# Kernel optimization log

Measured on AMD Instinct MI355X. Metric: run time of the kernel, lower is better.

## Reference

```python
import jax, jax.numpy as jnp
import numpy as np

N_LAYERS = 8
WIDTH = 1024
N = N_LAYERS * WIDTH


def setup_inputs() -> dict:
    key = jax.random.key(0)
    k1, k2 = jax.random.split(key)
    x = jax.random.normal(k1, (WIDTH,), dtype=jnp.float32)
    # parameter_matrix: row i = weights over all N neurons + bias in column N
    params = jax.random.normal(k2, (N, N + 1), dtype=jnp.float32) * 0.1
    # Layered DAG adjacency: layer l -> layer l+1 fully connected.
    adj_np = np.zeros((N, N), dtype=bool)
    for l in range(N_LAYERS - 1):
        adj_np[l * WIDTH:(l + 1) * WIDTH, (l + 1) * WIDTH:(l + 2) * WIDTH] = True
    return {"x": x, "params": params, "adj": jnp.asarray(adj_np)}


def reference(x, params, adj):
    """Faithful forward of connex NeuralNetwork with dropout_p=0.

    values starts at zero; input neurons (ids 0..W-1) are set to x.
    Each topological batch (= layer here) fires via the dense masked
    dot-product the original uses: dot(params[i,:N], values*adj[:,i]) + bias.
    Hidden neurons use silu, output neurons use identity.
    """
    n = params.shape[0]
    w = x.shape[0]
    n_layers = n // w
    values = jnp.zeros((n,), dtype=x.dtype).at[:w].set(x)
    for l in range(1, n_layers):  # static loop over topo batches
        lo, hi = l * w, (l + 1) * w
        mask = adj[:, lo:hi].T                      # (w, n) incoming-edge mask
        masked = jnp.where(mask, values[None, :], 0.0)
        pre = jnp.einsum('wn,wn->w', params[lo:hi, :n], masked) + params[lo:hi, n]
        out = pre if l == n_layers - 1 else jax.nn.silu(pre)  # output_activation = identity
        values = values.at[lo:hi].set(out)
    return values[-w:]
```

## Files before the change

### kernel.cpp

```cpp
#include <hip/hip_runtime.h>
#include <hip/hip_cooperative_groups.h>
#include <math.h>

#define W_    1024
#define NL_   8
#define NTOT_ (W_ * NL_)
#define RS_   (NTOT_ + 1)
#define NBLK  256

#define WS_BARRIER_OFF 2048

__device__ __forceinline__ void grid_barrier(unsigned* counter, unsigned* gen) {
    __syncthreads();
    if (threadIdx.x == 0) {
        unsigned g = __hip_atomic_load(gen, __ATOMIC_RELAXED, __HIP_MEMORY_SCOPE_AGENT);
        __threadfence();
        unsigned arrived = __hip_atomic_fetch_add(counter, 1u, __ATOMIC_ACQ_REL,
                                                  __HIP_MEMORY_SCOPE_AGENT);
        if (arrived == NBLK - 1) {
            __hip_atomic_store(counter, 0u, __ATOMIC_RELAXED, __HIP_MEMORY_SCOPE_AGENT);
            __hip_atomic_store(gen, g + 1u, __ATOMIC_RELEASE, __HIP_MEMORY_SCOPE_AGENT);
        } else {
            while (__hip_atomic_load(gen, __ATOMIC_RELAXED, __HIP_MEMORY_SCOPE_AGENT) == g)
                __builtin_amdgcn_s_sleep(1);
        }
        __threadfence();
    }
    __syncthreads();
}

__global__ __launch_bounds__(256, 1)
void mlp_fused(const float* __restrict__ x, const float* __restrict__ params,
               float* __restrict__ out, float* __restrict__ ws) {
    __shared__ float h[W_];
    const int tid  = threadIdx.x;
    const int lane = tid & 63;
    const int wave = tid >> 6;
    const int row  = blockIdx.x * 4 + wave;

    unsigned* counter = (unsigned*)(ws + WS_BARRIER_OFF);
    unsigned* gen     = (unsigned*)(ws + WS_BARRIER_OFF + 32);
    float* bufs[2] = { ws, ws + W_ };

    float xv[4];
#pragma unroll
    for (int i = 0; i < 4; ++i) xv[i] = x[tid + 256 * i];

    float w[NL_ - 1][16];
    float b[NL_ - 1];
#pragma unroll
    for (int l = 1; l < NL_; ++l) {
        const float* wrow = params + (size_t)(l * W_ + row) * RS_
                                   + (size_t)(l - 1) * W_ + lane;
#pragma unroll
        for (int i = 0; i < 16; ++i)
            w[l - 1][i] = wrow[64 * i];
        b[l - 1] = params[(size_t)(l * W_ + row) * RS_ + NTOT_];
    }

#pragma unroll
    for (int i = 0; i < 4; ++i) h[tid + 256 * i] = xv[i];
    __syncthreads();

#pragma unroll
    for (int l = 1; l < NL_; ++l) {
        if (l > 1) {
            grid_barrier(counter, gen);
            const float* cur = bufs[l & 1];
#pragma unroll
            for (int i = 0; i < 4; ++i) h[tid + 256 * i] = cur[tid + 256 * i];
            __syncthreads();
        }
        float acc = 0.f;
#pragma unroll
        for (int i = 0; i < 16; ++i)
            acc += w[l - 1][i] * h[lane + 64 * i];
#pragma unroll
        for (int off = 32; off; off >>= 1)
            acc += __shfl_down(acc, off);
        if (lane == 0) {
            float pre = acc + b[l - 1];
            if (l == NL_ - 1) out[row] = pre;
            else bufs[(l - 1) & 1][row] = pre / (1.f + __expf(-pre));
        }
    }
}

__global__ void init_vals(const float* __restrict__ x, float* __restrict__ buf) {
    int g = blockIdx.x * blockDim.x + threadIdx.x;
    if (g < W_) buf[g] = x[g];
}

__global__ __launch_bounds__(256)
void mlp_layer(const float* __restrict__ params, const float* __restrict__ in,
               float* __restrict__ outv, int l) {
    __shared__ float h[W_];
    const int tid  = threadIdx.x;
    const int lane = tid & 63;
    const int wave = tid >> 6;
    const int row  = blockIdx.x * 4 + wave;
#pragma unroll
    for (int i = 0; i < W_ / 256; ++i)
        h[tid + 256 * i] = in[tid + 256 * i];
    __syncthreads();
    const float* wrow = params + (size_t)(l * W_ + row) * RS_ + (size_t)(l - 1) * W_;
    float acc = 0.f;
#pragma unroll
    for (int i = 0; i < 16; ++i)
        acc += wrow[lane + 64 * i] * h[lane + 64 * i];
#pragma unroll
    for (int off = 32; off; off >>= 1)
        acc += __shfl_down(acc, off);
    if (lane == 0) {
        float pre = acc + params[(size_t)(l * W_ + row) * RS_ + NTOT_];
        float v = (l == NL_ - 1) ? pre : pre / (1.f + __expf(-pre));
        outv[row] = v;
    }
}

extern "C" void kernel_launch(void* const* d_in, const int* in_sizes, int n_in,
                              void* d_out, int out_size, void* d_ws, size_t ws_size,
                              hipStream_t stream) {
    const float* x      = (const float*)d_in[0];
    const float* params = (const float*)d_in[1];
    float* out = (float*)d_out;
    float* ws  = (float*)d_ws;

    hipMemsetAsync(ws + WS_BARRIER_OFF, 0, 256, stream);

    void* args[] = { (void*)&x, (void*)&params, (void*)&out, (void*)&ws };
    hipError_t err = hipLaunchCooperativeKernel((void*)mlp_fused,
                                                dim3(NBLK), dim3(256),
                                                args, 0, stream);
    if (err != hipSuccess) {
        float* buf0 = ws;
        float* buf1 = ws + W_;
        hipLaunchKernelGGL(init_vals, dim3(4), dim3(256), 0, stream, x, buf0);
        const float* cur = buf0;
        for (int l = 1; l < NL_; ++l) {
            float* dst = (l == NL_ - 1) ? out : ((cur == buf0) ? buf1 : buf0);
            hipLaunchKernelGGL(mlp_layer, dim3(256), dim3(256), 0, stream,
                               params, cur, dst, l);
            cur = dst;
        }
    }
}
```

Before: 497.7 us.

## Replace grid barrier with per-layer block flags and prefetch next-layer weights

Swaps the centralized atomic-counter grid barrier for per-layer, per-block ready flags. Each block polls all 256 flags in parallel using __syncthreads_and, so there is no contention on a single counter. Weight loading changes from all seven layers up front to a double-buffered register prefetch of the next layer, issued right after the flag is published. Activations are written and read with relaxed agent-scope atomics to bypass non-coherent caches, which adds flag memory and per-thread polling traffic.

```diff
diff --git a/kernel.cpp b/kernel.cpp
--- a/kernel.cpp
+++ b/kernel.cpp
@@ -8,25 +8,13 @@
 #define RS_   (NTOT_ + 1)
 #define NBLK  256
 
-#define WS_BARRIER_OFF 2048
+#define FLAGS_OFF 4096
 
-__device__ __forceinline__ void grid_barrier(unsigned* counter, unsigned* gen) {
-    __syncthreads();
-    if (threadIdx.x == 0) {
-        unsigned g = __hip_atomic_load(gen, __ATOMIC_RELAXED, __HIP_MEMORY_SCOPE_AGENT);
-        __threadfence();
-        unsigned arrived = __hip_atomic_fetch_add(counter, 1u, __ATOMIC_ACQ_REL,
-                                                  __HIP_MEMORY_SCOPE_AGENT);
-        if (arrived == NBLK - 1) {
-            __hip_atomic_store(counter, 0u, __ATOMIC_RELAXED, __HIP_MEMORY_SCOPE_AGENT);
-            __hip_atomic_store(gen, g + 1u, __ATOMIC_RELEASE, __HIP_MEMORY_SCOPE_AGENT);
-        } else {
-            while (__hip_atomic_load(gen, __ATOMIC_RELAXED, __HIP_MEMORY_SCOPE_AGENT) == g)
-                __builtin_amdgcn_s_sleep(1);
-        }
-        __threadfence();
-    }
-    __syncthreads();
+__device__ __forceinline__ float ld_bypass(const float* p) {
+    return __hip_atomic_load(p, __ATOMIC_RELAXED, __HIP_MEMORY_SCOPE_AGENT);
+}
+__device__ __forceinline__ void st_bypass(float* p, float v) {
+    __hip_atomic_store(p, v, __ATOMIC_RELAXED, __HIP_MEMORY_SCOPE_AGENT);
 }
 
 __global__ __launch_bounds__(256, 1)
@@ -38,50 +26,75 @@
     const int wave = tid >> 6;
     const int row  = blockIdx.x * 4 + wave;
 
-    unsigned* counter = (unsigned*)(ws + WS_BARRIER_OFF);
-    unsigned* gen     = (unsigned*)(ws + WS_BARRIER_OFF + 32);
+    unsigned* flags = (unsigned*)(ws + FLAGS_OFF);
     float* bufs[2] = { ws, ws + W_ };
+
+    float bias[NL_ - 1];
+#pragma unroll
+    for (int l = 1; l < NL_; ++l)
+        bias[l - 1] = params[(size_t)(l * W_ + row) * RS_ + NTOT_];
+
+    float wreg[2][16];
+    {
+        const float* wrow = params + (size_t)(1 * W_ + row) * RS_ + 0 * W_ + lane;
+#pragma unroll
+        for (int i = 0; i < 16; ++i) wreg[0][i] = wrow[64 * i];
+    }
 
     float xv[4];
 #pragma unroll
     for (int i = 0; i < 4; ++i) xv[i] = x[tid + 256 * i];
-
-    float w[NL_ - 1][16];
-    float b[NL_ - 1];
-#pragma unroll
-    for (int l = 1; l < NL_; ++l) {
-        const float* wrow = params + (size_t)(l * W_ + row) * RS_
-                                   + (size_t)(l - 1) * W_ + lane;
-#pragma unroll
-        for (int i = 0; i < 16; ++i)
-            w[l - 1][i] = wrow[64 * i];
-        b[l - 1] = params[(size_t)(l * W_ + row) * RS_ + NTOT_];
-    }
-
 #pragma unroll
     for (int i = 0; i < 4; ++i) h[tid + 256 * i] = xv[i];
     __syncthreads();
 
 #pragma unroll
     for (int l = 1; l < NL_; ++l) {
+        const int pb = (l - 1) & 1;
+
         if (l > 1) {
-            grid_barrier(counter, gen);
+            const unsigned* flg = flags + (size_t)(l - 2) * 256;
+            unsigned f;
+            do {
+                f = __hip_atomic_load(flg + tid, __ATOMIC_RELAXED,
+                                      __HIP_MEMORY_SCOPE_AGENT);
+            } while (!__syncthreads_and((int)(f != 0)));
+
             const float* cur = bufs[l & 1];
+            float hv[4];
 #pragma unroll
-            for (int i = 0; i < 4; ++i) h[tid + 256 * i] = cur[tid + 256 * i];
+            for (int i = 0; i < 4; ++i) hv[i] = ld_bypass(cur + tid + 256 * i);
+#pragma unroll
+            for (int i = 0; i < 4; ++i) h[tid + 256 * i] = hv[i];
             __syncthreads();
         }
+
         float acc = 0.f;
 #pragma unroll
         for (int i = 0; i < 16; ++i)
-            acc += w[l - 1][i] * h[lane + 64 * i];
+            acc += wreg[pb][i] * h[lane + 64 * i];
 #pragma unroll
         for (int off = 32; off; off >>= 1)
             acc += __shfl_down(acc, off);
+
         if (lane == 0) {
-            float pre = acc + b[l - 1];
+            float pre = acc + bias[l - 1];
             if (l == NL_ - 1) out[row] = pre;
-            else bufs[(l - 1) & 1][row] = pre / (1.f + __expf(-pre));
+            else st_bypass(bufs[(l - 1) & 1] + row,
+                           pre / (1.f + __expf(-pre)));
+        }
+
+        if (l < NL_ - 1) {
+            __syncthreads();
+            if (tid == 0)
+                __hip_atomic_store(flags + (size_t)(l - 1) * 256 + blockIdx.x,
+                                   1u, __ATOMIC_RELEASE, __HIP_MEMORY_SCOPE_AGENT);
+            if (l < NL_ - 2 + 1) {
+                const float* wrow = params + (size_t)((l + 1) * W_ + row) * RS_
+                                           + (size_t)l * W_ + lane;
+#pragma unroll
+                for (int i = 0; i < 16; ++i) wreg[l & 1][i] = wrow[64 * i];
+            }
         }
     }
 }
@@ -126,7 +139,7 @@
     float* out = (float*)d_out;
     float* ws  = (float*)d_ws;
 
-    hipMemsetAsync(ws + WS_BARRIER_OFF, 0, 256, stream);
+    hipMemsetAsync(ws + FLAGS_OFF, 0, 6 * 256 * sizeof(unsigned), stream);
 
     void* args[] = { (void*)&x, (void*)&params, (void*)&out, (void*)&ws };
     hipError_t err = hipLaunchCooperativeKernel((void*)mlp_fused,
```

New measurement: 477.2 us. -4.1%, faster.
